# Kernel optimization log

Hardware: AMD Instinct MI355X
Metric: run time of the kernel (lower is better)

## Reference

```python
import jax, jax.numpy as jnp
import numpy as np
import math

B, S, D, H, DFF, V = 8, 512, 512, 8, 2048, 32000
EPS = 1e-5

def _pe_table(max_len, d):
    pos = jnp.arange(max_len, dtype=jnp.float32)[:, None]
    i = jnp.arange(d)
    exponent = (2 * (i // 2)).astype(jnp.float32) / d
    angle = pos / jnp.power(10000.0, exponent)[None, :]
    return jnp.where(i % 2 == 0, jnp.sin(angle), jnp.cos(angle))

def _ln(x, g, b):
    mu = jnp.mean(x, -1, keepdims=True)
    var = jnp.mean((x - mu) ** 2, -1, keepdims=True)
    return g * (x - mu) * jax.lax.rsqrt(var + EPS) + b

def setup_inputs() -> dict:
    key = jax.random.key(0)
    ks = jax.random.split(key, 16)
    n = jax.random.normal
    return {
        "tokens": jax.random.randint(ks[0], (B, S), 0, V, dtype=jnp.int32),
        "emb": n(ks[1], (V, D), jnp.float32),
        "pe": _pe_table(1000, D),
        "Wq": n(ks[2], (H, D, D), jnp.float32), "bq": jnp.zeros((H, D), jnp.float32),
        "Wk": n(ks[3], (H, D, D), jnp.float32), "bk": jnp.zeros((H, D), jnp.float32),
        "Wv": n(ks[4], (H, D, D), jnp.float32), "bv": jnp.zeros((H, D), jnp.float32),
        "Wo": n(ks[5], (H * D, D), jnp.float32), "bo": jnp.zeros((D,), jnp.float32),
        "g1": jnp.ones((D,), jnp.float32), "be1": jnp.zeros((D,), jnp.float32),
        "W1": n(ks[6], (D, DFF), jnp.float32), "b1": jnp.zeros((DFF,), jnp.float32),
        "W2": n(ks[7], (DFF, D), jnp.float32), "b2": jnp.zeros((D,), jnp.float32),
        "g2": jnp.ones((D,), jnp.float32), "be2": jnp.zeros((D,), jnp.float32),
        "Wf": n(ks[8], (D, V), jnp.float32), "bf": jnp.zeros((V,), jnp.float32),
    }

def reference(tokens, emb, pe, Wq, bq, Wk, bk, Wv, bv, Wo, bo, g1, be1,
              W1, b1, W2, b2, g2, be2, Wf, bf):
    x = emb[tokens] + pe[:tokens.shape[1]]  # [B,S,D]
    res = x
    # input-level "causal" mask over (seq, feature) plane, as in the source
    mask = jnp.triu(jnp.ones((S, D), dtype=bool), k=1)
    xm = jnp.where(mask, 0.0, x)
    scale = 1.0 / math.sqrt(D)
    q = jnp.einsum('bsd,hde->hbse', xm, Wq) + bq[:, None, None, :]
    k = jnp.einsum('bsd,hde->hbse', xm, Wk) + bk[:, None, None, :]
    v = jnp.einsum('bsd,hde->hbse', xm, Wv) + bv[:, None, None, :]
    attn = jax.nn.softmax(jnp.einsum('hbse,hbte->hbst', q, k) * scale, axis=-1)
    o = jnp.einsum('hbst,hbte->hbse', attn, v)  # [H,B,S,D]
    cat = o.transpose(1, 2, 0, 3).reshape(B, S, H * D)  # matches torch.cat head order
    x = _ln(res + (cat @ Wo + bo), g1, be1)
    res = x
    ff = jax.nn.relu(x @ W1 + b1) @ W2 + b2
    x = _ln(res + ff, g2, be2)
    return x @ Wf + bf  # [B,S,V]
```

## Files before the change

### kernel.cpp

```cpp
#include <hip/hip_runtime.h>

typedef unsigned short u16;
typedef unsigned int u32;
typedef short s16x8 __attribute__((ext_vector_type(8)));
typedef __bf16 bf16x8 __attribute__((ext_vector_type(8)));
typedef float f32x4 __attribute__((ext_vector_type(4)));

#define DEVI static __device__ __forceinline__

#define SS 512
#define DD 512
#define NFF 2048
#define VV 32000
#define MTOT 4096
#define HD 4096
#define KC 1536

DEVI float bf2f(u16 h){ return __uint_as_float(((u32)h) << 16); }
DEVI u16 f2bf(float f){
  u32 u = __float_as_uint(f);
  return (u16)((u + 0x7FFFu + ((u >> 16) & 1u)) >> 16);
}
DEVI float ldf(const void* p, long i, int isbf){
  return isbf ? bf2f(((const u16*)p)[i]) : ((const float*)p)[i];
}

DEVI f32x4 mfma16(s16x8 a, s16x8 b, f32x4 c){
  return __builtin_amdgcn_mfma_f32_16x16x32_bf16(
      __builtin_bit_cast(bf16x8, a), __builtin_bit_cast(bf16x8, b), c, 0, 0, 0);
}

typedef const __attribute__((address_space(1))) unsigned int* gup;
typedef __attribute__((address_space(3))) unsigned int* lup;
DEVI void gload16(const void* g, void* l){
  __builtin_amdgcn_global_load_lds((gup)g, (lup)l, 16, 0, 0);
}

DEVI float wave_redsum(float v){
  #pragma unroll
  for (int off = 32; off > 0; off >>= 1) v += __shfl_xor(v, off, 64);
  return v;
}

__global__ void k_dflag(const void* pe, int* flag){
  flag[0] = (*(const u32*)pe == 0x3F800000u) ? 1 : 0;
}

__global__ __launch_bounds__(256) void k_embed(
    const int* __restrict__ tok, const void* __restrict__ emb, const void* __restrict__ pe,
    float* __restrict__ x, u16* __restrict__ xm2, const int* __restrict__ dflag)
{
  int isbf = dflag[0];
  int blk = blockIdx.x;
  int s = blk & (SS - 1);
  int t = tok[blk];
  long rb = (long)blk * 1024;
  for (int d = threadIdx.x; d < DD; d += 256){
    float e = ldf(emb, (long)t * DD + d, isbf) + ldf(pe, (long)s * DD + d, isbf);
    x[(long)blk * DD + d] = e;
    float m = (d <= s) ? e : 0.f;
    u16 hi = f2bf(m);
    u16 lo = f2bf(m - bf2f(hi));
    xm2[rb + d] = hi;
    xm2[rb + 512 + d] = lo;
  }
}

__global__ __launch_bounds__(256) void k_wsplitT(
    const void* __restrict__ Wq, const void* __restrict__ Wk,
    u16* __restrict__ Wq2, u16* __restrict__ Wk2, const int* __restrict__ dflag)
{
  int isbf = dflag[0];
  int zz = blockIdx.z;
  const void* in = (zz < 8) ? Wq : Wk;
  u16* out = (zz < 8) ? Wq2 : Wk2;
  int z = zz & 7;
  long zin = (long)z * DD * DD;
  long zout = (long)z * DD * 1024;
  __shared__ float t[32][33];
  int e0 = blockIdx.x * 32, d0 = blockIdx.y * 32;
  int tx = threadIdx.x & 31, ty = threadIdx.x >> 5;
  #pragma unroll
  for (int i = 0; i < 4; i++){
    int d = ty + i * 8;
    t[d][tx] = ldf(in, zin + (long)(d0 + d) * DD + e0 + tx, isbf);
  }
  __syncthreads();
  #pragma unroll
  for (int i = 0; i < 4; i++){
    int e = ty + i * 8;
    float v = t[tx][e];
    u16 hi = f2bf(v);
    u16 lo = f2bf(v - bf2f(hi));
    long ob = zout + (long)(e0 + e) * 1024 + d0 + tx;
    out[ob] = hi;
    out[ob + 512] = lo;
  }
}

__global__ __launch_bounds__(256) void k_transAll(
    const void* __restrict__ Wv, const void* __restrict__ Wo,
    const void* __restrict__ W1, const void* __restrict__ W2,
    const void* __restrict__ Wf,
    u16* __restrict__ WvT, u16* __restrict__ WoT, u16* __restrict__ W1T,
    u16* __restrict__ W2T, u16* __restrict__ WfT, const int* __restrict__ dflag)
{
  int isbf = dflag[0];
  int f = blockIdx.x;
  const void* in; u16* out; int R, C, gx, loc;
  if (f < 2048)      { in = Wv; out = WvT; R = 512;  C = 512;   gx = 16;   loc = f; }
  else if (f < 4096) { in = Wo; out = WoT; R = 4096; C = 512;   gx = 16;   loc = f - 2048; }
  else if (f < 5120) { in = W1; out = W1T; R = 512;  C = 2048;  gx = 64;   loc = f - 4096; }
  else if (f < 6144) { in = W2; out = W2T; R = 2048; C = 512;   gx = 16;   loc = f - 5120; }
  else               { in = Wf; out = WfT; R = 512;  C = 32000; gx = 1000; loc = f - 6144; }
  int bx = loc % gx;
  int rest = loc / gx;
  int gy = R >> 5;
  int by = rest % gy, z = rest / gy;
  long zo = (long)z * R * C;
  __shared__ float t[32][33];
  int c0 = bx * 32, r0 = by * 32;
  int tx = threadIdx.x & 31, ty = threadIdx.x >> 5;
  #pragma unroll
  for (int i = 0; i < 4; i++){
    int r = ty + i * 8;
    t[r][tx] = ldf(in, zo + (long)(r0 + r) * C + c0 + tx, isbf);
  }
  __syncthreads();
  #pragma unroll
  for (int i = 0; i < 4; i++){
    int c = ty + i * 8;
    out[zo + (long)(c0 + c) * R + r0 + tx] = f2bf(t[tx][c]);
  }
}

enum { EP_QK = 0, EP_SCALE = 1, EP_VT = 2, EP_CAT = 3, EP_OUT = 4,
       EP_F32RES = 5, EP_RELU = 6 };

template<int MODE, bool GSWAP>
__global__ __launch_bounds__(256) void k_mfma(
    const u16* __restrict__ A, long sA, int lda,
    const u16* __restrict__ Bt, long sB,
    void* __restrict__ Cv,
    const void* __restrict__ bias,
    const float* __restrict__ res,
    int K, int ldc, float scale,
    const int* __restrict__ dflag)
{
  int isbf = dflag[0];
  int z = blockIdx.z;
  const u16* Ab = A + (long)z * sA;
  const u16* Bb = Bt + (long)z * sB;
  __shared__ __align__(16) u16 As[2][4][128][8];
  __shared__ __align__(16) u16 Bs[2][4][128][8];
  int m0 = (GSWAP ? blockIdx.x : blockIdx.y) * 128;
  int n0 = (GSWAP ? blockIdx.y : blockIdx.x) * 128;
  int tid = threadIdx.x;
  int lane = tid & 63, w = tid >> 6;
  int wr = (w >> 1) * 64, wc = (w & 1) * 64;
  int l15 = lane & 15, l4 = lane >> 4;
  int s0 = w * 64 + lane;
  int ar0 = s0 & 127, ak0 = s0 >> 7;
  int ak1 = ak0 + 2;
  f32x4 zero = {0.f, 0.f, 0.f, 0.f};
  f32x4 acc[4][4];
  #pragma unroll
  for (int i = 0; i < 4; i++)
    #pragma unroll
    for (int j = 0; j < 4; j++) acc[i][j] = zero;

  const long arow0 = (long)(m0 + ar0) * lda;
  const long brow0 = (long)(n0 + ar0) * K;

  #define STAGE(buf, k0) do{ \
    u16* AsF = &As[buf][0][0][0]; \
    u16* BsF = &Bs[buf][0][0][0]; \
    gload16(Ab + arow0 + (k0) + ak0 * 8, AsF + (long)(w * 64) * 8); \
    gload16(Ab + arow0 + (k0) + ak1 * 8, AsF + (long)(256 + w * 64) * 8); \
    gload16(Bb + brow0 + (k0) + ak0 * 8, BsF + (long)(w * 64) * 8); \
    gload16(Bb + brow0 + (k0) + ak1 * 8, BsF + (long)(256 + w * 64) * 8); \
  }while(0)

  #define COMPUTE(buf) do{ \
    s16x8 af[4], bfr[4]; \
    _Pragma("unroll") \
    for (int i = 0; i < 4; i++) af[i] = *(const s16x8*)&As[buf][l4][wr + i * 16 + l15][0]; \
    _Pragma("unroll") \
    for (int j = 0; j < 4; j++) bfr[j] = *(const s16x8*)&Bs[buf][l4][wc + j * 16 + l15][0]; \
    _Pragma("unroll") \
    for (int i = 0; i < 4; i++) \
      _Pragma("unroll") \
      for (int j = 0; j < 4; j++) \
        acc[i][j] = mfma16(af[i], bfr[j], acc[i][j]); \
  }while(0)

  STAGE(0, 0);
  __syncthreads();
  for (int k0 = 0; k0 < K; k0 += 64){
    STAGE(1, k0 + 32);
    COMPUTE(0);
    __syncthreads();
    if (k0 + 64 < K) STAGE(0, k0 + 64);
    COMPUTE(1);
    __syncthreads();
  }
  #undef STAGE
  #undef COMPUTE

  int mbase = m0 + wr + l4 * 4;
  int nbase = n0 + wc + l15;
  if constexpr (MODE == EP_F32RES){
    float* C = (float*)Cv;
    #pragma unroll
    for (int j = 0; j < 4; j++){
      int n = nbase + j * 16;
      float badd = ldf(bias, n, isbf);
      #pragma unroll
      for (int i = 0; i < 4; i++)
        #pragma unroll
        for (int r = 0; r < 4; r++){
          long a = (long)(mbase + i * 16 + r) * ldc + n;
          C[a] = acc[i][j][r] + badd + res[a];
        }
    }
  } else if constexpr (MODE == EP_RELU){
    u16* C = (u16*)Cv;
    #pragma unroll
    for (int j = 0; j < 4; j++){
      int n = nbase + j * 16;
      float badd = ldf(bias, n, isbf);
      #pragma unroll
      for (int i = 0; i < 4; i++)
        #pragma unroll
        for (int r = 0; r < 4; r++)
          C[(long)(mbase + i * 16 + r) * ldc + n] = f2bf(fmaxf(acc[i][j][r] + badd, 0.f));
    }
  }
}

template<int MODE, bool GSWAP, int AMAP, int BMAP>
__global__ __launch_bounds__(512, 2) void k_mfma2(
    const u16* __restrict__ A, long sA, int lda,
    const u16* __restrict__ Bt, long sB, int ldb,
    void* __restrict__ Cv,
    const void* __restrict__ bias,
    const float* __restrict__ res,
    int K, int ldc, float scale,
    const int* __restrict__ dflag)
{
  int isbf = dflag[0];
  int z = blockIdx.z;
  const u16* Ab = A + (long)z * sA;
  const u16* Bb = Bt + (long)z * sB;
  __shared__ __align__(16) char smem[65536];
  u16* SA = (u16*)smem;
  u16* SB = (u16*)(smem + 32768);
  int m0, n0;
  if constexpr (GSWAP){
    int f = blockIdx.x + gridDim.x * blockIdx.y;
    int q = (gridDim.x * gridDim.y) >> 3;
    int L = (f & 7) * q + (f >> 3);
    m0 = (L % gridDim.x) * 256;
    n0 = (L / gridDim.x) * 256;
  } else {
    m0 = blockIdx.y * 256;
    n0 = blockIdx.x * 256;
  }
  int tid = threadIdx.x;
  int lane = tid & 63, w = tid >> 6;
  int wm = (w >> 2) * 128, wn = (w & 3) * 64;
  int l15 = lane & 15, l4 = lane >> 4;
  int row = tid & 255, ob = tid >> 8;
  f32x4 zero = {0.f, 0.f, 0.f, 0.f};
  f32x4 acc[8][4];
  #pragma unroll
  for (int i = 0; i < 8; i++)
    #pragma unroll
    for (int j = 0; j < 4; j++) acc[i][j] = zero;

  const long arow0 = (long)(m0 + row) * lda;
  const long brow0 = (long)(n0 + row) * ldb;

  #define STAGE2(buf, k0_) do{ \
    int ka = (AMAP == 1) ? ((k0_) < 512 ? (k0_) : (k0_) - 512) \
           : (AMAP == 2) ? ((k0_) < 1024 ? (k0_) : (k0_) - 1024) : (k0_); \
    int kb = (BMAP == 1) ? ((k0_) < 512 ? (k0_) : (k0_) - 512) \
           : (BMAP == 2) ? ((k0_) < 1024 ? (k0_) : (k0_) - 1024) : (k0_); \
    gload16(Ab + arow0 + ka + ob * 8,       SA + ((buf) * 8192 + (ob * 256 + row) * 8)); \
    gload16(Ab + arow0 + ka + (ob + 2) * 8, SA + ((buf) * 8192 + ((ob + 2) * 256 + row) * 8)); \
    gload16(Bb + brow0 + kb + ob * 8,       SB + ((buf) * 8192 + (ob * 256 + row) * 8)); \
    gload16(Bb + brow0 + kb + (ob + 2) * 8, SB + ((buf) * 8192 + ((ob + 2) * 256 + row) * 8)); \
  }while(0)

  #define COMPUTE2(buf) do{ \
    s16x8 bfr[4]; \
    _Pragma("unroll") \
    for (int j = 0; j < 4; j++) \
      bfr[j] = *(const s16x8*)(SB + ((buf) * 8192 + l4 * 2048 + (wn + j * 16 + l15) * 8)); \
    _Pragma("unroll") \
    for (int i = 0; i < 8; i++){ \
      s16x8 af = *(const s16x8*)(SA + ((buf) * 8192 + l4 * 2048 + (wm + i * 16 + l15) * 8)); \
      _Pragma("unroll") \
      for (int j = 0; j < 4; j++) \
        acc[i][j] = mfma16(af, bfr[j], acc[i][j]); \
    } \
  }while(0)

  STAGE2(0, 0);
  __syncthreads();
  for (int k0 = 0; k0 < K; k0 += 64){
    STAGE2(1, k0 + 32);
    COMPUTE2(0);
    __syncthreads();
    if (k0 + 64 < K) STAGE2(0, k0 + 64);
    COMPUTE2(1);
    __syncthreads();
  }
  #undef STAGE2
  #undef COMPUTE2

  int mbase = m0 + wm + l4 * 4;
  int nbase = n0 + wn + l15;
  if constexpr (MODE == EP_CAT){
    u16* C = (u16*)Cv;
    int h = z >> 3, b = z & 7;
    #pragma unroll
    for (int i = 0; i < 8; i++){
      int s = mbase + i * 16;
      #pragma unroll
      for (int j = 0; j < 4; j++){
        int n = nbase + j * 16;
        #pragma unroll
        for (int r = 0; r < 4; r++)
          C[((long)b * SS + s + r) * HD + (long)h * DD + n] = f2bf(acc[i][j][r]);
      }
    }
  } else if constexpr (MODE == EP_OUT){
    float* O = (float*)Cv;
    float* ldsT = (float*)smem;
    const int RST = 260;
    int hs16 = (w >> 2) * 16;
    float badd[4];
    #pragma unroll
    for (int j = 0; j < 4; j++) badd[j] = ldf(bias, n0 + wn + j * 16 + l15, isbf);
    #pragma unroll
    for (int i = 0; i < 8; i++){
      __syncthreads();
      #pragma unroll
      for (int j = 0; j < 4; j++){
        int col = wn + j * 16 + l15;
        #pragma unroll
        for (int r = 0; r < 4; r++)
          ldsT[(hs16 + l4 * 4 + r) * RST + col] = acc[i][j][r] + badd[j];
      }
      __syncthreads();
      #pragma unroll
      for (int p = 0; p < 4; p++){
        int chunk = tid + p * 512;
        int lr = chunk >> 6, c4 = chunk & 63;
        int gm = m0 + (lr >> 4) * 128 + i * 16 + (lr & 15);
        f32x4 v = *(f32x4*)&ldsT[lr * RST + c4 * 4];
        __builtin_nontemporal_store(v, (f32x4*)&O[(long)gm * ldc + n0 + c4 * 4]);
      }
    }
  }
}

__global__ __launch_bounds__(512, 2) void k_proj(
    const u16* __restrict__ xm2,
    const u16* __restrict__ Wq2, const u16* __restrict__ Wk2, const u16* __restrict__ WvT,
    u16* __restrict__ q2, u16* __restrict__ k2, u16* __restrict__ vT,
    const void* __restrict__ bq, const void* __restrict__ bk, const void* __restrict__ bv,
    const int* __restrict__ dflag)
{
  int isbf = dflag[0];
  int zz = blockIdx.z;
  int z, ldb, K, amap, bmap, mode;
  const u16* Bb; const void* bias; u16* C;
  if (zz < 16){
    mode = 0; z = zz & 7;
    Bb = (zz < 8 ? Wq2 : Wk2) + (long)z * 524288;
    ldb = 1024; K = KC; amap = 1; bmap = 2;
    bias = (zz < 8) ? bq : bk;
    C = (zz < 8) ? q2 : k2;
  } else {
    mode = 1; z = zz - 16;
    Bb = WvT + (long)z * 262144;
    ldb = 512; K = 512; amap = 0; bmap = 0;
    bias = bv;
    C = vT;
  }
  const u16* Ab = xm2;
  __shared__ __align__(16) char smem[65536];
  u16* SA = (u16*)smem;
  u16* SB = (u16*)(smem + 32768);
  int m0 = blockIdx.y * 256;
  int n0 = blockIdx.x * 256;
  int tid = threadIdx.x;
  int lane = tid & 63, w = tid >> 6;
  int wm = (w >> 2) * 128, wn = (w & 3) * 64;
  int l15 = lane & 15, l4 = lane >> 4;
  int row = tid & 255, ob = tid >> 8;
  f32x4 zero = {0.f, 0.f, 0.f, 0.f};
  f32x4 acc[8][4];
  #pragma unroll
  for (int i = 0; i < 8; i++)
    #pragma unroll
    for (int j = 0; j < 4; j++) acc[i][j] = zero;

  const long arow0 = (long)(m0 + row) * 1024;
  const long brow0 = (long)(n0 + row) * ldb;

  #define STAGEP(buf, k0_) do{ \
    int ka = (amap == 1) ? ((k0_) < 512 ? (k0_) : (k0_) - 512) : (k0_); \
    int kb = (bmap == 2) ? ((k0_) < 1024 ? (k0_) : (k0_) - 1024) : (k0_); \
    gload16(Ab + arow0 + ka + ob * 8,       SA + ((buf) * 8192 + (ob * 256 + row) * 8)); \
    gload16(Ab + arow0 + ka + (ob + 2) * 8, SA + ((buf) * 8192 + ((ob + 2) * 256 + row) * 8)); \
    gload16(Bb + brow0 + kb + ob * 8,       SB + ((buf) * 8192 + (ob * 256 + row) * 8)); \
    gload16(Bb + brow0 + kb + (ob + 2) * 8, SB + ((buf) * 8192 + ((ob + 2) * 256 + row) * 8)); \
  }while(0)

  #define COMPUTEP(buf) do{ \
    s16x8 bfr[4]; \
    _Pragma("unroll") \
    for (int j = 0; j < 4; j++) \
      bfr[j] = *(const s16x8*)(SB + ((buf) * 8192 + l4 * 2048 + (wn + j * 16 + l15) * 8)); \
    _Pragma("unroll") \
    for (int i = 0; i < 8; i++){ \
      s16x8 af = *(const s16x8*)(SA + ((buf) * 8192 + l4 * 2048 + (wm + i * 16 + l15) * 8)); \
      _Pragma("unroll") \
      for (int j = 0; j < 4; j++) \
        acc[i][j] = mfma16(af, bfr[j], acc[i][j]); \
    } \
  }while(0)

  STAGEP(0, 0);
  __syncthreads();
  for (int k0 = 0; k0 < K; k0 += 64){
    STAGEP(1, k0 + 32);
    COMPUTEP(0);
    __syncthreads();
    if (k0 + 64 < K) STAGEP(0, k0 + 64);
    COMPUTEP(1);
    __syncthreads();
  }
  #undef STAGEP
  #undef COMPUTEP

  int mbase = m0 + wm + l4 * 4;
  int nbase = n0 + wn + l15;
  if (mode == 0){
    u16* Cz = C + (long)z * ((long)MTOT * 1024);
    #pragma unroll
    for (int j = 0; j < 4; j++){
      int n = nbase + j * 16;
      float badd = ldf(bias, (long)z * DD + n, isbf);
      #pragma unroll
      for (int i = 0; i < 8; i++)
        #pragma unroll
        for (int r = 0; r < 4; r++){
          float qv = acc[i][j][r] + badd;
          u16 hi = f2bf(qv);
          u16 lo = f2bf(qv - bf2f(hi));
          long rb = (long)(mbase + i * 16 + r) * 1024;
          Cz[rb + n] = hi;
          Cz[rb + 512 + n] = lo;
        }
    }
  } else {
    #pragma unroll
    for (int i = 0; i < 8; i++){
      int mrow = mbase + i * 16;
      int b = mrow >> 9, s = mrow & (SS - 1);
      #pragma unroll
      for (int j = 0; j < 4; j++){
        int n = nbase + j * 16;
        float badd = ldf(bias, (long)z * DD + n, isbf);
        ushort4 pk;
        pk.x = f2bf(acc[i][j][0] + badd); pk.y = f2bf(acc[i][j][1] + badd);
        pk.z = f2bf(acc[i][j][2] + badd); pk.w = f2bf(acc[i][j][3] + badd);
        *(ushort4*)&C[((long)(z * 8 + b) * DD + n) * SS + s] = pk;
      }
    }
  }
}

template<int AMAP, int BMAP>
__global__ __launch_bounds__(512, 2) void k_fsm(
    const u16* __restrict__ A, long sA, int lda,
    const u16* __restrict__ Bt, long sB, int ldb,
    u16* __restrict__ P, int K, float scale,
    const int* __restrict__ dflag)
{
  int z = blockIdx.z;
  const u16* Ab = A + (long)z * sA;
  const u16* Bb = Bt + (long)z * sB;
  __shared__ __align__(16) char smem[81920];
  u16* SA = (u16*)smem;
  u16* SB = (u16*)(smem + 16384);
  int m0 = blockIdx.x * 128;
  int tid = threadIdx.x;
  int lane = tid & 63, w = tid >> 6;
  int wn = w * 64;
  int l15 = lane & 15, l4 = lane >> 4;
  f32x4 zero = {0.f, 0.f, 0.f, 0.f};
  f32x4 acc[8][4];
  #pragma unroll
  for (int i = 0; i < 8; i++)
    #pragma unroll
    for (int j = 0; j < 4; j++) acc[i][j] = zero;

  const long arow0 = (long)(m0 + (tid & 127)) * lda;
  const int akc = tid >> 7;
  const long brow0 = (long)tid * ldb;

  #define STAGEF(buf, k0_) do{ \
    int ka = (AMAP == 1) ? ((k0_) < 512 ? (k0_) : (k0_) - 512) \
           : (AMAP == 2) ? ((k0_) < 1024 ? (k0_) : (k0_) - 1024) : (k0_); \
    int kb = (BMAP == 1) ? ((k0_) < 512 ? (k0_) : (k0_) - 512) \
           : (BMAP == 2) ? ((k0_) < 1024 ? (k0_) : (k0_) - 1024) : (k0_); \
    gload16(Ab + arow0 + ka + akc * 8, SA + ((buf) * 4096 + tid * 8)); \
    gload16(Bb + brow0 + kb + 0,  SB + ((buf) * 16384 + (0 * 512 + tid) * 8)); \
    gload16(Bb + brow0 + kb + 8,  SB + ((buf) * 16384 + (1 * 512 + tid) * 8)); \
    gload16(Bb + brow0 + kb + 16, SB + ((buf) * 16384 + (2 * 512 + tid) * 8)); \
    gload16(Bb + brow0 + kb + 24, SB + ((buf) * 16384 + (3 * 512 + tid) * 8)); \
  }while(0)

  #define COMPUTEF(buf) do{ \
    s16x8 bfr[4]; \
    _Pragma("unroll") \
    for (int j = 0; j < 4; j++) \
      bfr[j] = *(const s16x8*)(SB + ((buf) * 16384 + l4 * 4096 + (wn + j * 16 + l15) * 8)); \
    _Pragma("unroll") \
    for (int i = 0; i < 8; i++){ \
      s16x8 af = *(const s16x8*)(SA + ((buf) * 4096 + l4 * 1024 + (i * 16 + l15) * 8)); \
      _Pragma("unroll") \
      for (int j = 0; j < 4; j++) \
        acc[i][j] = mfma16(af, bfr[j], acc[i][j]); \
    } \
  }while(0)

  STAGEF(0, 0);
  __syncthreads();
  for (int k0 = 0; k0 < K; k0 += 64){
    STAGEF(1, k0 + 32);
    COMPUTEF(0);
    __syncthreads();
    if (k0 + 64 < K) STAGEF(0, k0 + 64);
    COMPUTEF(1);
    __syncthreads();
  }
  #undef STAGEF
  #undef COMPUTEF

  float* sred = (float*)smem;
  float* srow = (float*)(smem + 4096);

  #pragma unroll
  for (int i = 0; i < 8; i++)
    #pragma unroll
    for (int j = 0; j < 4; j++)
      acc[i][j] *= scale;

  #pragma unroll
  for (int i = 0; i < 8; i++)
    #pragma unroll
    for (int r = 0; r < 4; r++){
      float m = fmaxf(fmaxf(acc[i][0][r], acc[i][1][r]),
                      fmaxf(acc[i][2][r], acc[i][3][r]));
      #pragma unroll
      for (int off = 1; off < 16; off <<= 1) m = fmaxf(m, __shfl_xor(m, off, 64));
      if (l15 == 0) sred[w * 128 + l4 * 4 + i * 16 + r] = m;
    }
  __syncthreads();
  if (tid < 128){
    float m = sred[tid];
    #pragma unroll
    for (int w2 = 1; w2 < 8; w2++) m = fmaxf(m, sred[w2 * 128 + tid]);
    srow[tid] = m;
  }
  __syncthreads();
  #pragma unroll
  for (int i = 0; i < 8; i++)
    #pragma unroll
    for (int r = 0; r < 4; r++){
      float rm = srow[l4 * 4 + i * 16 + r];
      float s = 0.f;
      #pragma unroll
      for (int j = 0; j < 4; j++){
        float e = expf(acc[i][j][r] - rm);
        acc[i][j][r] = e;
        s += e;
      }
      #pragma unroll
      for (int off = 1; off < 16; off <<= 1) s += __shfl_xor(s, off, 64);
      if (l15 == 0) sred[w * 128 + l4 * 4 + i * 16 + r] = s;
    }
  __syncthreads();
  if (tid < 128){
    float s = 0.f;
    #pragma unroll
    for (int w2 = 0; w2 < 8; w2++) s += sred[w2 * 128 + tid];
    srow[tid] = 1.f / s;
  }
  __syncthreads();
  u16* Pz = P + (long)z * ((long)SS * SS);
  u16* pb = (u16*)(smem + 8192);
  const int PST = 520;
  #pragma unroll
  for (int ii = 0; ii < 4; ii++){
    __syncthreads();
    #pragma unroll
    for (int s2 = 0; s2 < 2; s2++){
      int i = ii * 2 + s2;
      #pragma unroll
      for (int r = 0; r < 4; r++){
        int rl = l4 * 4 + i * 16 + r;
        float inv = srow[rl];
        #pragma unroll
        for (int j = 0; j < 4; j++)
          pb[(s2 * 16 + l4 * 4 + r) * PST + wn + j * 16 + l15] = f2bf(acc[i][j][r] * inv);
      }
    }
    __syncthreads();
    #pragma unroll
    for (int p = 0; p < 8; p++){
      int chunk = tid + p * 512;
      int lr = chunk >> 7, c8 = chunk & 127;
      ushort4 v = *(ushort4*)&pb[lr * PST + c8 * 4];
      *(ushort4*)&Pz[(long)(m0 + ii * 32 + lr) * SS + c8 * 4] = v;
    }
  }
}

template<bool WF32>
__global__ __launch_bounds__(256) void k_ln(
    const float* __restrict__ X, const void* __restrict__ g, const void* __restrict__ be,
    u16* __restrict__ Yb, float* __restrict__ Yf, const int* __restrict__ dflag)
{
  int isbf = dflag[0];
  int row = blockIdx.x * 4 + (threadIdx.x >> 6);
  int lane = threadIdx.x & 63;
  const float* p = X + (long)row * DD + lane * 8;
  float4 v0 = *(const float4*)p;
  float4 v1 = *(const float4*)(p + 4);
  float v[8] = {v0.x, v0.y, v0.z, v0.w, v1.x, v1.y, v1.z, v1.w};
  float s = 0.f;
  #pragma unroll
  for (int i = 0; i < 8; i++) s += v[i];
  s = wave_redsum(s);
  float mu = s * (1.f / DD);
  float d_[8], sq = 0.f;
  #pragma unroll
  for (int i = 0; i < 8; i++){ d_[i] = v[i] - mu; sq += d_[i] * d_[i]; }
  sq = wave_redsum(sq);
  float rs = 1.f / sqrtf(sq * (1.f / DD) + 1e-5f);
  #pragma unroll
  for (int i = 0; i < 8; i++){
    int dd = lane * 8 + i;
    float y = ldf(g, dd, isbf) * d_[i] * rs + ldf(be, dd, isbf);
    Yb[(long)row * DD + dd] = f2bf(y);
    if (WF32) Yf[(long)row * DD + dd] = y;
  }
}

extern "C" void kernel_launch(void* const* d_in, const int* in_sizes, int n_in,
                              void* d_out, int out_size, void* d_ws, size_t ws_size,
                              hipStream_t stream)
{
  const int* tokens = (const int*)d_in[0];
  const void* emb = d_in[1];
  const void* pe  = d_in[2];
  const void* Wq  = d_in[3];
  const void* bq  = d_in[4];
  const void* Wk  = d_in[5];
  const void* bk  = d_in[6];
  const void* Wv  = d_in[7];
  const void* bv  = d_in[8];
  const void* Wo  = d_in[9];
  const void* bo  = d_in[10];
  const void* g1  = d_in[11];
  const void* be1 = d_in[12];
  const void* W1  = d_in[13];
  const void* b1  = d_in[14];
  const void* W2  = d_in[15];
  const void* b2  = d_in[16];
  const void* g2  = d_in[17];
  const void* be2 = d_in[18];
  const void* Wf  = d_in[19];
  const void* bfb = d_in[20];
  float* out = (float*)d_out;
  char* ws = (char*)d_ws;
  char* DO = (char*)d_out;

  const size_t MB = 1ull << 20;
  int* dflag = (int*)ws;
  u16* x2b   = (u16*)(ws + 1 * MB);
  u16* WfT   = (u16*)(ws + 8 * MB);

  float* x    = (float*)(DO + 0 * MB);
  u16*   xm2  = (u16*)(DO + 8 * MB);
  u16*   Wq2  = (u16*)(DO + 16 * MB);
  u16*   Wk2  = (u16*)(DO + 24 * MB);
  u16*   WvT  = (u16*)(DO + 32 * MB);
  u16*   WoT  = (u16*)(DO + 36 * MB);
  u16*   W1T  = (u16*)(DO + 40 * MB);
  u16*   W2T  = (u16*)(DO + 42 * MB);
  u16*   q2   = (u16*)(DO + 48 * MB);
  u16*   k2   = (u16*)(DO + 112 * MB);
  u16*   attn = (u16*)(DO + 240 * MB);
  u16*   vT   = (u16*)(DO + 272 * MB);
  u16*   cat  = (u16*)(DO + 304 * MB);
  float* proj = (float*)(DO + 336 * MB);
  float* x1f  = (float*)(DO + 344 * MB);
  u16*   x1b  = (u16*)(DO + 352 * MB);
  u16*   ff1  = (u16*)(DO + 356 * MB);
  float* ff2  = (float*)(DO + 372 * MB);

  const float scale = 0.04419417382415922f;
  const long HSL = 262144;
  const long QSL = 524288;

  k_dflag<<<1, 1, 0, stream>>>(pe, dflag);
  k_embed<<<dim3(4096), 256, 0, stream>>>(tokens, emb, pe, x, xm2, dflag);

  k_wsplitT<<<dim3(16, 16, 16), 256, 0, stream>>>(Wq, Wk, Wq2, Wk2, dflag);
  k_transAll<<<dim3(22144), 256, 0, stream>>>(
      Wv, Wo, W1, W2, Wf, WvT, WoT, W1T, W2T, WfT, dflag);

  k_proj<<<dim3(2, 16, 24), 512, 0, stream>>>(
      xm2, Wq2, Wk2, WvT, q2, k2, vT, bq, bk, bv, dflag);

  k_fsm<1, 2><<<dim3(4, 1, 64), 512, 0, stream>>>(
      q2, QSL, 1024, k2, QSL, 1024, attn, KC, scale, dflag);

  k_mfma2<EP_CAT, false, 0, 0><<<dim3(2, 2, 64), 512, 0, stream>>>(
      attn, HSL, SS, vT, HSL, 512, cat, nullptr, nullptr, SS, 0, 0.f, dflag);

  k_mfma<EP_F32RES, false><<<dim3(4, 32, 1), 256, 0, stream>>>(
      cat, 0, HD, WoT, 0, proj, bo, x, HD, DD, 0.f, dflag);
  k_ln<true><<<dim3(1024), 256, 0, stream>>>(proj, g1, be1, x1b, x1f, dflag);

  k_mfma<EP_RELU, false><<<dim3(16, 32, 1), 256, 0, stream>>>(
      x1b, 0, DD, W1T, 0, ff1, b1, nullptr, DD, NFF, 0.f, dflag);
  k_mfma<EP_F32RES, false><<<dim3(4, 32, 1), 256, 0, stream>>>(
      ff1, 0, NFF, W2T, 0, ff2, b2, x1f, NFF, DD, 0.f, dflag);
  k_ln<false><<<dim3(1024), 256, 0, stream>>>(ff2, g2, be2, x2b, nullptr, dflag);

  k_mfma2<EP_OUT, true, 0, 0><<<dim3(16, 125, 1), 512, 0, stream>>>(
      x2b, 0, DD, WfT, 0, 512, out, bfb, nullptr, DD, VV, 0.f, dflag);
}
```

Baseline: 1.003 ms.

## Add dedicated double-buffered MFMA kernel for final vocab projection

Replaces the generic k_mfma2 output-projection path with a specialized kernel, k_out8. It uses 128KB LDS double buffering with async global-to-LDS loads for the next K-tile issued while MFMAs run on the current one, plus split waitcnt/barrier scheduling and setprio around the MFMA bursts. The K=512 loop is hard-coded as 8 tiles of 64. The generic kernel's grid swizzle is simplified and moved into the new kernel. The goal is to hide memory latency in the largest GEMM. The 128KB LDS per block may limit occupancy despite launch_bounds(512,2).

```diff
diff --git a/kernel.cpp b/kernel.cpp
--- a/kernel.cpp
+++ b/kernel.cpp
@@ -255,17 +255,8 @@
   __shared__ __align__(16) char smem[65536];
   u16* SA = (u16*)smem;
   u16* SB = (u16*)(smem + 32768);
-  int m0, n0;
-  if constexpr (GSWAP){
-    int f = blockIdx.x + gridDim.x * blockIdx.y;
-    int q = (gridDim.x * gridDim.y) >> 3;
-    int L = (f & 7) * q + (f >> 3);
-    m0 = (L % gridDim.x) * 256;
-    n0 = (L / gridDim.x) * 256;
-  } else {
-    m0 = blockIdx.y * 256;
-    n0 = blockIdx.x * 256;
-  }
+  int m0 = (GSWAP ? blockIdx.x : blockIdx.y) * 256;
+  int n0 = (GSWAP ? blockIdx.y : blockIdx.x) * 256;
   int tid = threadIdx.x;
   int lane = tid & 63, w = tid >> 6;
   int wm = (w >> 2) * 128, wn = (w & 3) * 64;
@@ -335,33 +326,110 @@
           C[((long)b * SS + s + r) * HD + (long)h * DD + n] = f2bf(acc[i][j][r]);
       }
     }
-  } else if constexpr (MODE == EP_OUT){
-    float* O = (float*)Cv;
-    float* ldsT = (float*)smem;
-    const int RST = 260;
-    int hs16 = (w >> 2) * 16;
-    float badd[4];
-    #pragma unroll
-    for (int j = 0; j < 4; j++) badd[j] = ldf(bias, n0 + wn + j * 16 + l15, isbf);
-    #pragma unroll
-    for (int i = 0; i < 8; i++){
-      __syncthreads();
-      #pragma unroll
-      for (int j = 0; j < 4; j++){
-        int col = wn + j * 16 + l15;
+  }
+}
+
+__global__ __launch_bounds__(512, 2) void k_out8(
+    const u16* __restrict__ A, const u16* __restrict__ Bt,
+    float* __restrict__ O, const void* __restrict__ bias,
+    int NT, const int* __restrict__ dflag)
+{
+  int isbf = dflag[0];
+  __shared__ __align__(16) char smem[131072];
+  u16* SM = (u16*)smem;
+  int f = blockIdx.x + gridDim.x * blockIdx.y;
+  int qx = (gridDim.x * gridDim.y) >> 3;
+  int L = (f & 7) * qx + (f >> 3);
+  int m0 = (L % gridDim.x) * 256;
+  int n0 = (L / gridDim.x) * 256;
+  int tid = threadIdx.x;
+  int lane = tid & 63, w = tid >> 6;
+  int wm = (w >> 2) * 128, wn = (w & 3) * 64;
+  int l15 = lane & 15, l4 = lane >> 4;
+  f32x4 zero = {0.f, 0.f, 0.f, 0.f};
+  f32x4 acc[8][4];
+  #pragma unroll
+  for (int i = 0; i < 8; i++)
+    #pragma unroll
+    for (int j = 0; j < 4; j++) acc[i][j] = zero;
+
+  int rr = tid & 127, kc1 = tid >> 7;
+
+  #define STAGEU(c, Tt, u) do{ \
+    const u16* gb = (((u) & 1) == 0) ? A : Bt; \
+    int base0 = (((u) & 1) == 0) ? m0 : n0; \
+    int r2 = ((u) >> 1) * 128 + rr; \
+    long gsrc = (long)(base0 + r2) * 512 + (Tt) * 64; \
+    u16* lb = SM + (c) * 32768 + ((((u) & 1) == 0) ? 0 : 16384); \
+    gload16(gb + gsrc + kc1 * 8,       lb + (kc1 * 256 + r2) * 8); \
+    gload16(gb + gsrc + (kc1 + 4) * 8, lb + ((kc1 + 4) * 256 + r2) * 8); \
+  }while(0)
+
+  STAGEU(0, 0, 0); STAGEU(0, 0, 1); STAGEU(0, 0, 2); STAGEU(0, 0, 3);
+
+  int cur = 0;
+  for (int T = 0; T < NT; T++){
+    int nxt = cur ^ 1;
+    int more = (T + 1 < NT);
+    s16x8 af[8];
+    #pragma unroll
+    for (int q = 0; q < 4; q++){
+      if (more) STAGEU(nxt, T + 1, q);
+      if (q == 0){
+        if (more) asm volatile("s_waitcnt vmcnt(2)" ::: "memory");
+        else      asm volatile("s_waitcnt vmcnt(0)" ::: "memory");
+      }
+      __builtin_amdgcn_s_barrier();
+      __builtin_amdgcn_sched_barrier(0);
+      int ks = q >> 1, jh = q & 1;
+      if (jh == 0){
         #pragma unroll
-        for (int r = 0; r < 4; r++)
-          ldsT[(hs16 + l4 * 4 + r) * RST + col] = acc[i][j][r] + badd[j];
+        for (int i = 0; i < 8; i++)
+          af[i] = *(const s16x8*)(SM + cur * 32768 +
+                    ((ks * 4 + l4) * 256 + (wm + i * 16 + l15)) * 8);
       }
-      __syncthreads();
-      #pragma unroll
-      for (int p = 0; p < 4; p++){
-        int chunk = tid + p * 512;
-        int lr = chunk >> 6, c4 = chunk & 63;
-        int gm = m0 + (lr >> 4) * 128 + i * 16 + (lr & 15);
-        f32x4 v = *(f32x4*)&ldsT[lr * RST + c4 * 4];
-        __builtin_nontemporal_store(v, (f32x4*)&O[(long)gm * ldc + n0 + c4 * 4]);
+      s16x8 b0 = *(const s16x8*)(SM + cur * 32768 + 16384 +
+                    ((ks * 4 + l4) * 256 + (wn + (jh * 2) * 16 + l15)) * 8);
+      s16x8 b1 = *(const s16x8*)(SM + cur * 32768 + 16384 +
+                    ((ks * 4 + l4) * 256 + (wn + (jh * 2 + 1) * 16 + l15)) * 8);
+      __builtin_amdgcn_s_setprio(1);
+      #pragma unroll
+      for (int i = 0; i < 8; i++){
+        acc[i][jh * 2]     = mfma16(af[i], b0, acc[i][jh * 2]);
+        acc[i][jh * 2 + 1] = mfma16(af[i], b1, acc[i][jh * 2 + 1]);
       }
+      __builtin_amdgcn_s_setprio(0);
+    }
+    __builtin_amdgcn_s_barrier();
+    __builtin_amdgcn_sched_barrier(0);
+    cur = nxt;
+  }
+  #undef STAGEU
+
+  float* ldsT = (float*)smem;
+  const int RST = 260;
+  int hs16 = (w >> 2) * 16;
+  float badd[4];
+  #pragma unroll
+  for (int j = 0; j < 4; j++) badd[j] = ldf(bias, n0 + wn + j * 16 + l15, isbf);
+  #pragma unroll
+  for (int i = 0; i < 8; i++){
+    __syncthreads();
+    #pragma unroll
+    for (int j = 0; j < 4; j++){
+      int col = wn + j * 16 + l15;
+      #pragma unroll
+      for (int r = 0; r < 4; r++)
+        ldsT[(hs16 + l4 * 4 + r) * RST + col] = acc[i][j][r] + badd[j];
+    }
+    __syncthreads();
+    #pragma unroll
+    for (int p = 0; p < 4; p++){
+      int chunk = tid + p * 512;
+      int lr = chunk >> 6, c4 = chunk & 63;
+      int gm = m0 + (lr >> 4) * 128 + i * 16 + (lr & 15);
+      f32x4 v = *(f32x4*)&ldsT[lr * RST + c4 * 4];
+      __builtin_nontemporal_store(v, (f32x4*)&O[(long)gm * VV + n0 + c4 * 4]);
     }
   }
 }
@@ -747,6 +815,5 @@
       ff1, 0, NFF, W2T, 0, ff2, b2, x1f, NFF, DD, 0.f, dflag);
   k_ln<false><<<dim3(1024), 256, 0, stream>>>(ff2, g2, be2, x2b, nullptr, dflag);
 
-  k_mfma2<EP_OUT, true, 0, 0><<<dim3(16, 125, 1), 512, 0, stream>>>(
-      x2b, 0, DD, WfT, 0, 512, out, bfb, nullptr, DD, VV, 0.f, dflag);
-}
+  k_out8<<<dim3(16, 125, 1), 512, 0, stream>>>(x2b, WfT, out, bfb, 8, dflag);
+}
```

Result: faster. 970.4 us (-3.2%).
